# Kernel optimization log

Hardware: AMD Instinct MI355X
Metric: run time of the kernel (lower is better)

Reference implementation:

```python
import jax, jax.numpy as jnp
import numpy as np

N = 50000      # nodes
E = 1600000    # edges (avg degree 32)
F_IN = 512     # num_node_features
NHID = 128     # args.nhid
NCLS = 64      # num_classes


def _gcn_conv(x, W, b, src, dst):
    """PyG GCNConv with symmetric normalization and self-loops.
    x' = D^{-1/2} (A + I) D^{-1/2} (x W) + b, D = degree of (A + I)."""
    h = x @ W                                   # [N, d_out] linear first
    ones = jnp.ones(src.shape[0], h.dtype)
    deg = jnp.zeros(N, h.dtype).at[dst].add(ones) + 1.0  # +1 for self-loop
    dinv = jax.lax.rsqrt(deg)                   # D^{-1/2}
    norm = dinv[src] * dinv[dst]                # per-edge coefficient
    msg = h[src] * norm[:, None]                # gather + scale  [E, d_out]
    agg = jnp.zeros_like(h).at[dst].add(msg)    # scatter-add
    agg = agg + h * (dinv * dinv)[:, None]      # self-loop term (norm = dinv_i^2)
    return agg + b


def setup_inputs() -> dict:
    key = jax.random.key(0)
    k0, k1, k2, k3, k4, k5 = jax.random.split(key, 6)
    x = jax.random.normal(k0, (N, F_IN), jnp.float32)
    edge_index = jax.random.randint(k1, (2, E), 0, N, jnp.int32)
    W1 = jax.random.normal(k2, (F_IN, NHID), jnp.float32) / np.sqrt(F_IN)
    b1 = jnp.zeros((NHID,), jnp.float32)
    W2 = jax.random.normal(k3, (NHID, NCLS), jnp.float32) / np.sqrt(NHID)
    b2 = jnp.zeros((NCLS,), jnp.float32)
    return {"x": x, "edge_index": edge_index, "W1": W1, "b1": b1, "W2": W2, "b2": b2}


def reference(x, edge_index, W1, b1, W2, b2):
    src, dst = edge_index[0], edge_index[1]
    h = jax.nn.relu(_gcn_conv(x, W1, b1, src, dst))
    # dropout is identity at inference (training=False)
    out = _gcn_conv(h, W2, b2, src, dst)
    return jax.nn.softmax(out, axis=1)
```

## Files before the change

### kernel.cpp

```cpp
#include <hip/hip_runtime.h>
#include <hip/hip_bf16.h>
#include <hip/hip_fp16.h>


#define F_IN 512
#define NHID 128
#define NCLS 64
#define BSHIFT 8
#define CHUNK 4096
#define BM 64
#define BK 32

typedef __attribute__((ext_vector_type(8))) short short8;
typedef __attribute__((ext_vector_type(4))) float f32x4;

__device__ __forceinline__ unsigned f2u(float f) { union { float f; unsigned u; } v; v.f = f; return v.u; }
__device__ __forceinline__ float u2f(unsigned u) { union { unsigned u; float f; } v; v.u = u; return v.f; }


__global__ __launch_bounds__(256) void bin_kernel(const int* __restrict__ src,
        const int* __restrict__ dst, unsigned* __restrict__ pairs,
        int* __restrict__ bcur, int E, int cap) {
    __shared__ int lcnt[256];
    __shared__ int lscan[256];
    __shared__ int gbase[256];
    __shared__ int wsum[4];
    __shared__ unsigned stage[CHUNK];
    const int t = threadIdx.x;
    const int lane = t & 63, wid = t >> 6;
    const int e0 = blockIdx.x * CHUNK;
    const int n = min(CHUNK, E - e0);

    lcnt[t] = 0;
    __syncthreads();
    for (int i = t; i < n; i += 256)
        atomicAdd(&lcnt[dst[e0 + i] >> BSHIFT], 1);
    __syncthreads();
    const int v = lcnt[t];
    int s = v;
    #pragma unroll
    for (int d = 1; d < 64; d <<= 1) {
        int tt = __shfl_up(s, d);
        if (lane >= d) s += tt;
    }
    if (lane == 63) wsum[wid] = s;
    __syncthreads();
    int woff = 0;
    for (int w = 0; w < wid; ++w) woff += wsum[w];
    lscan[t] = woff + s - v;
    gbase[t] = v ? atomicAdd(&bcur[t], v) : 0;
    lcnt[t] = 0;
    __syncthreads();
    for (int i = t; i < n; i += 256) {
        unsigned d = (unsigned)dst[e0 + i], sc = (unsigned)src[e0 + i];
        int b = d >> BSHIFT;
        int p = atomicAdd(&lcnt[b], 1);
        stage[lscan[b] + p] = (d << 16) | sc;
    }
    __syncthreads();
    for (int i = t; i < n; i += 256) {
        unsigned pr = stage[i];
        int b = pr >> 24;
        int off = gbase[b] + (i - lscan[b]);
        if (off < cap) pairs[(size_t)b * cap + off] = pr;
    }
}


__global__ __launch_bounds__(256) void scanB_kernel(const int* __restrict__ bcur,
        int* __restrict__ bbase, int nbuck, int cap) {
    __shared__ int wsum[4];
    const int t = threadIdx.x;
    const int lane = t & 63, wid = t >> 6;
    int v = (t < nbuck) ? min(bcur[t], cap) : 0;
    int s = v;
    #pragma unroll
    for (int d = 1; d < 64; d <<= 1) {
        int tt = __shfl_up(s, d);
        if (lane >= d) s += tt;
    }
    if (lane == 63) wsum[wid] = s;
    __syncthreads();
    int woff = 0;
    for (int w = 0; w < wid; ++w) woff += wsum[w];
    bbase[t] = woff + s - v;
}


__global__ __launch_bounds__(512) void countscan_b_kernel(
        const unsigned* __restrict__ pairs, const int* __restrict__ bcur,
        const int* __restrict__ bbase, int* __restrict__ row_ptr,
        float* __restrict__ dinv, int cap, int N) {
    __shared__ int hist[256];
    __shared__ int wsum[4];
    const int b = blockIdx.x;
    const int t = threadIdx.x;
    if (t < 256) hist[t] = 0;
    __syncthreads();
    const int n = min(bcur[b], cap);
    const unsigned* p = pairs + (size_t)b * cap;
    for (int i = t; i < n; i += 512)
        atomicAdd(&hist[(p[i] >> 16) & 255], 1);
    __syncthreads();
    if (t < 256) {
        const int lane = t & 63, wid = t >> 6;
        const int v = hist[t];
        int s = v;
        #pragma unroll
        for (int d = 1; d < 64; d <<= 1) {
            int tt = __shfl_up(s, d);
            if (lane >= d) s += tt;
        }
        if (lane == 63) wsum[wid] = s;
        __syncthreads();
        int woff = 0;
        for (int w = 0; w < wid; ++w) woff += wsum[w];
        const int excl = woff + s - v;
        const int node = (b << BSHIFT) + t;
        if (node <= N) row_ptr[node] = bbase[b] + excl;
        if (node < N) dinv[node] = rsqrtf((float)v + 1.0f);
    }
}


__global__ __launch_bounds__(1024) void fill_b_kernel(const unsigned* __restrict__ pairs,
        const int* __restrict__ bcur, const int* __restrict__ row_ptr,
        int* __restrict__ col, int cap) {
    __shared__ int lcur[256];
    const int b = blockIdx.x;
    const int t = threadIdx.x;
    if (t < 256) lcur[t] = 0;
    __syncthreads();
    const int n = min(bcur[b], cap);
    const unsigned* p = pairs + (size_t)b * cap;
    for (int i = t; i < n; i += 1024) {
        unsigned pr = p[i];
        int dl = (pr >> 16) & 255;
        int pos = row_ptr[(b << BSHIFT) + dl] + atomicAdd(&lcur[dl], 1);
        col[pos] = (int)(pr & 0xffffu);
    }
}


__global__ __launch_bounds__(256) void prepW_kernel(const float* __restrict__ W1,
        short* __restrict__ Wp) {
    const int g = blockIdx.x * 256 + threadIdx.x;
    const int f = g >> 6;
    const int lane = g & 63;
    const int ks = f >> 3, nt = f & 7;
    const int colg = nt * 16 + (lane & 15);
    const int k0 = ks * 32 + (lane >> 4) * 8;
    short8 vb;
    #pragma unroll
    for (int j = 0; j < 8; ++j) {
        unsigned u = f2u(W1[(size_t)(k0 + j) * NHID + colg]);
        unsigned r = (u + 0x7fffu + ((u >> 16) & 1u)) >> 16;
        vb[j] = (short)r;
    }
    *reinterpret_cast<short8*>(Wp + ((size_t)f << 9) + (lane << 3)) = vb;
}


__device__ __forceinline__ void cvt8v(const f32x4& u0, const f32x4& u1,
                                      short8& h, short8& l) {
    float av[8] = {u0[0], u0[1], u0[2], u0[3], u1[0], u1[1], u1[2], u1[3]};
    #pragma unroll
    for (int j = 0; j < 8; ++j) {
        unsigned u = f2u(av[j]);
        h[j] = (short)(u >> 16);
        float hif = u2f(u & 0xffff0000u);
        l[j] = (short)(f2u(av[j] - hif) >> 16);
    }
}

#define STAGE(bufidx, ksv) do { \
    const char* _xb = (const char*)X + (size_t)(ksv) * 128; \
    char* _ab = (char*)&Abuf[bufidx][0] + tid * 16; \
    __builtin_amdgcn_global_load_lds((const unsigned*)(_xb + aoff0), (unsigned*)(_ab),        16, 0, 0); \
    __builtin_amdgcn_global_load_lds((const unsigned*)(_xb + aoff1), (unsigned*)(_ab + 4096), 16, 0, 0); \
    const char* _wb = (const char*)Wp + (size_t)(ksv) * 8192 + tid * 16; \
    char* _bb = (char*)&Bbuf[bufidx][0] + tid * 16; \
    __builtin_amdgcn_global_load_lds((const unsigned*)(_wb),        (unsigned*)(_bb),        16, 0, 0); \
    __builtin_amdgcn_global_load_lds((const unsigned*)(_wb + 4096), (unsigned*)(_bb + 4096), 16, 0, 0); \
} while (0)

__global__ __launch_bounds__(256, 4) void gemm1_mfma(
        const float* __restrict__ X, const short* __restrict__ Wp,
        const float* __restrict__ dinv, __half* __restrict__ Hs16, int M) {
    __shared__ float Abuf[2][BM * BK];
    __shared__ short Bbuf[2][8 * 512];
    const int tid = threadIdx.x;
    const int lane = tid & 63;
    const int wid = tid >> 6;
    const int l15 = lane & 15;
    const int kc = lane >> 4;
    const int m0 = blockIdx.x * BM;

    int aoff0, aoff1;
    {
        int o, row, c, grow;
        o = tid * 16;        row = o >> 7; c = ((o >> 4) & 7) ^ (row & 7);
        grow = m0 + row; if (grow > M - 1) grow = M - 1; aoff0 = grow * 2048 + c * 16;
        o = 4096 + tid * 16; row = o >> 7; c = ((o >> 4) & 7) ^ (row & 7);
        grow = m0 + row; if (grow > M - 1) grow = M - 1; aoff1 = grow * 2048 + c * 16;
    }

    const int row0 = wid * 16 + l15;
    const int ra0 = row0 * 128 + (((kc * 2) ^ (row0 & 7)) * 16);
    const int ra1 = row0 * 128 + (((kc * 2 + 1) ^ (row0 & 7)) * 16);

    f32x4 acc[8];
    #pragma unroll
    for (int j = 0; j < 8; ++j)
        acc[j] = (f32x4){0.f, 0.f, 0.f, 0.f};

    STAGE(0, 0);
    __syncthreads();

    for (int ks = 0; ks < 16; ++ks) {
        const int cur = ks & 1;
        if (ks + 1 < 16) STAGE(cur ^ 1, ks + 1);
        const char* ab = (const char*)&Abuf[cur][0];
        const f32x4 x0 = *reinterpret_cast<const f32x4*>(ab + ra0);
        const f32x4 x1 = *reinterpret_cast<const f32x4*>(ab + ra1);
        short8 ah, al;
        cvt8v(x0, x1, ah, al);
        const char* bb = (const char*)&Bbuf[cur][0];
        short8 bfr[8];
        #pragma unroll
        for (int nt = 0; nt < 8; ++nt)
            bfr[nt] = *reinterpret_cast<const short8*>(bb + nt * 1024 + lane * 16);
        #pragma unroll
        for (int nt = 0; nt < 8; ++nt) {
            acc[nt] = __builtin_amdgcn_mfma_f32_16x16x32_bf16(ah, bfr[nt], acc[nt], 0, 0, 0);
            acc[nt] = __builtin_amdgcn_mfma_f32_16x16x32_bf16(al, bfr[nt], acc[nt], 0, 0, 0);
        }
        __syncthreads();
    }

    #pragma unroll
    for (int r = 0; r < 4; ++r) {
        const int orow = m0 + wid * 16 + kc * 4 + r;
        if (orow < M) {
            const float di = dinv[orow];
            #pragma unroll
            for (int nt = 0; nt < 8; ++nt) {
                Hs16[(size_t)orow * NHID + nt * 16 + l15] =
                    __float2half(acc[nt][r] * di);
            }
        }
    }
}


__global__ __launch_bounds__(64) void agg1_kernel(const __half2* __restrict__ Hs,
        const int* __restrict__ row_ptr, const int* __restrict__ col,
        const float* __restrict__ dinv, const float* __restrict__ b1,
        float* __restrict__ Y) {
    const int i = blockIdx.x;
    const int c = threadIdx.x;
    const int beg = row_ptr[i], end = row_ptr[i + 1];
    float2 f = __half22float2(Hs[(size_t)i * 64 + c]);
    float ax = f.x, ay = f.y;
    int e = beg;
    for (; e + 8 <= end; e += 8) {
        float2 v[8];
        #pragma unroll
        for (int j = 0; j < 8; ++j) {
            int s = col[e + j];
            v[j] = __half22float2(Hs[(size_t)s * 64 + c]);
        }
        #pragma unroll
        for (int j = 0; j < 8; ++j) { ax += v[j].x; ay += v[j].y; }
    }
    for (; e < end; ++e) {
        float2 v = __half22float2(Hs[(size_t)col[e] * 64 + c]);
        ax += v.x; ay += v.y;
    }
    const float di = dinv[i];
    const float2 bb = reinterpret_cast<const float2*>(b1)[c];
    float2 o;
    o.x = fmaxf(fmaf(ax, di, bb.x), 0.0f);
    o.y = fmaxf(fmaf(ay, di, bb.y), 0.0f);
    *reinterpret_cast<float2*>(&Y[(size_t)i * NHID + 2 * c]) = o;
}


__global__ __launch_bounds__(256) void gemm2_kernel(const float* __restrict__ Y,
        const float* __restrict__ W2, const float* __restrict__ dinv,
        __half* __restrict__ H2s16, int N) {
    __shared__ float Ws[NHID][NCLS];
    __shared__ float Ys[16][NHID];
    const int tid = threadIdx.x;
    const int i0 = blockIdx.x * 16;
    #pragma unroll
    for (int t = 0; t < 8; ++t) {
        int v = tid + t * 256;
        int k = v >> 4;
        int c4 = (v & 15) * 4;
        *reinterpret_cast<float4*>(&Ws[k][c4]) =
            *reinterpret_cast<const float4*>(&W2[(size_t)k * NCLS + c4]);
    }
    #pragma unroll
    for (int t = 0; t < 2; ++t) {
        int v = tid + t * 256;
        int r = v >> 5;
        int c4 = (v & 31) * 4;
        int gr = i0 + r; if (gr > N - 1) gr = N - 1;
        *reinterpret_cast<float4*>(&Ys[r][c4]) =
            *reinterpret_cast<const float4*>(&Y[(size_t)gr * NHID + c4]);
    }
    __syncthreads();
    const int c = tid & 63;
    const int rg = tid >> 6;
    float acc[4] = {0.f, 0.f, 0.f, 0.f};
    #pragma unroll 8
    for (int k = 0; k < NHID; ++k) {
        float w = Ws[k][c];
        #pragma unroll
        for (int j = 0; j < 4; ++j)
            acc[j] = fmaf(Ys[rg * 4 + j][k], w, acc[j]);
    }
    #pragma unroll
    for (int j = 0; j < 4; ++j) {
        int gr = i0 + rg * 4 + j;
        if (gr < N) H2s16[(size_t)gr * NCLS + c] = __float2half(acc[j] * dinv[gr]);
    }
}


__global__ __launch_bounds__(64) void agg2_kernel(const __half2* __restrict__ H2,
        const int* __restrict__ row_ptr, const int* __restrict__ col,
        const float* __restrict__ dinv, const float* __restrict__ b2,
        float* __restrict__ out, int N) {
    const int lane = threadIdx.x;
    const int node = blockIdx.x * 2 + (lane >> 5);
    const int c = lane & 31;
    if (node >= N) return;
    const int beg = row_ptr[node], end = row_ptr[node + 1];
    float2 f = __half22float2(H2[(size_t)node * 32 + c]);
    float ax = f.x, ay = f.y;
    int e = beg;
    for (; e + 8 <= end; e += 8) {
        float2 v[8];
        #pragma unroll
        for (int j = 0; j < 8; ++j) {
            int s = col[e + j];
            v[j] = __half22float2(H2[(size_t)s * 32 + c]);
        }
        #pragma unroll
        for (int j = 0; j < 8; ++j) { ax += v[j].x; ay += v[j].y; }
    }
    for (; e < end; ++e) {
        float2 v = __half22float2(H2[(size_t)col[e] * 32 + c]);
        ax += v.x; ay += v.y;
    }
    const float di = dinv[node];
    const float2 bb = reinterpret_cast<const float2*>(b2)[c];
    float vx = fmaf(ax, di, bb.x);
    float vy = fmaf(ay, di, bb.y);
    float m = fmaxf(vx, vy);
    #pragma unroll
    for (int d = 16; d >= 1; d >>= 1) m = fmaxf(m, __shfl_xor(m, d));
    float ex = __expf(vx - m), ey = __expf(vy - m);
    float sum = ex + ey;
    #pragma unroll
    for (int d = 16; d >= 1; d >>= 1) sum += __shfl_xor(sum, d);
    float2 o = {ex / sum, ey / sum};
    reinterpret_cast<float2*>(out)[(size_t)node * 32 + c] = o;
}


extern "C" void kernel_launch(void* const* d_in, const int* in_sizes, int n_in,
                              void* d_out, int out_size, void* d_ws, size_t ws_size,
                              hipStream_t stream) {
    const float* x  = (const float*)d_in[0];
    const int*   ei = (const int*)d_in[1];
    const float* W1 = (const float*)d_in[2];
    const float* b1 = (const float*)d_in[3];
    const float* W2 = (const float*)d_in[4];
    const float* b2 = (const float*)d_in[5];
    const int N = in_sizes[0] / F_IN;
    const int E = in_sizes[1] / 2;
    const int* src = ei;
    const int* dst = ei + E;
    float* out = (float*)d_out;

    const int Npad  = (N + 63) & ~63;
    const int Epad  = (E + 63) & ~63;
    int*      bcur    = (int*)d_ws;
    int*      bbase   = bcur + 256;
    int*      row_ptr = bbase + 256;
    float*    dinv    = (float*)(row_ptr + Npad);
    int*      col     = (int*)(dinv + Npad);
    __half*   Hs16    = (__half*)(col + Epad);
    float*    Y       = (float*)(Hs16 + (size_t)Npad * NHID);
    __half*   H2s16   = Hs16;
    short*    Wp      = (short*)Y;
    unsigned* pairs   = (unsigned*)((char*)Y + 512 * 1024);

    const int nbuck = (N + 255) >> BSHIFT;
    const int cap = (((E / nbuck) * 3 / 2) + 63) & ~63;

    hipMemsetAsync(bcur, 0, 256 * sizeof(int), stream);
    bin_kernel<<<(E + CHUNK - 1) / CHUNK, 256, 0, stream>>>(src, dst, pairs, bcur, E, cap);
    scanB_kernel<<<1, 256, 0, stream>>>(bcur, bbase, nbuck, cap);
    countscan_b_kernel<<<nbuck, 512, 0, stream>>>(pairs, bcur, bbase, row_ptr, dinv, cap, N);
    fill_b_kernel<<<nbuck, 1024, 0, stream>>>(pairs, bcur, row_ptr, col, cap);
    prepW_kernel<<<32, 256, 0, stream>>>(W1, Wp);
    gemm1_mfma<<<(N + BM - 1) / BM, 256, 0, stream>>>(x, Wp, dinv, Hs16, N);
    agg1_kernel<<<N, 64, 0, stream>>>((const __half2*)Hs16, row_ptr, col, dinv, b1, Y);
    gemm2_kernel<<<(N + 15) / 16, 256, 0, stream>>>(Y, W2, dinv, H2s16, N);
    agg2_kernel<<<(N + 1) / 2, 64, 0, stream>>>((const __half2*)H2s16, row_ptr, col, dinv, b2, out, N);
}
```

Before: 175.6 us.

## Fuse CSR bucket scan, count and fill; store hidden activations in fp16

Merges the bucket-offset scan, per-bucket count/scan and fill kernels into one kernel. Each block now computes its own bucket base with a reduction over earlier bucket counts and reuses the shared-memory scan for the column placement, which removes two launches and the global row_ptr reads. Separately, the layer-1 output Y is stored as half2 instead of fp32, halving the write and re-read traffic between agg1 and gemm2, at the cost of reduced precision. The workspace layout changes so that Y16, Wp and pairs no longer alias.

```diff
diff --git a/kernel.cpp b/kernel.cpp
--- a/kernel.cpp
+++ b/kernel.cpp
@@ -67,76 +67,62 @@
 }
 
 
-__global__ __launch_bounds__(256) void scanB_kernel(const int* __restrict__ bcur,
-        int* __restrict__ bbase, int nbuck, int cap) {
-    __shared__ int wsum[4];
-    const int t = threadIdx.x;
-    const int lane = t & 63, wid = t >> 6;
-    int v = (t < nbuck) ? min(bcur[t], cap) : 0;
-    int s = v;
-    #pragma unroll
-    for (int d = 1; d < 64; d <<= 1) {
-        int tt = __shfl_up(s, d);
-        if (lane >= d) s += tt;
-    }
-    if (lane == 63) wsum[wid] = s;
-    __syncthreads();
-    int woff = 0;
-    for (int w = 0; w < wid; ++w) woff += wsum[w];
-    bbase[t] = woff + s - v;
-}
-
-
-__global__ __launch_bounds__(512) void countscan_b_kernel(
+__global__ __launch_bounds__(1024) void countfill_b_kernel(
         const unsigned* __restrict__ pairs, const int* __restrict__ bcur,
-        const int* __restrict__ bbase, int* __restrict__ row_ptr,
-        float* __restrict__ dinv, int cap, int N) {
+        int* __restrict__ row_ptr, float* __restrict__ dinv,
+        int* __restrict__ col, int cap, int N) {
     __shared__ int hist[256];
+    __shared__ int lscan[256];
+    __shared__ int red[16];
     __shared__ int wsum[4];
     const int b = blockIdx.x;
     const int t = threadIdx.x;
+    const int lane = t & 63, wv = t >> 6;
+
+    int bv = (t < 256 && t < b) ? min(bcur[t], cap) : 0;
+    #pragma unroll
+    for (int d = 32; d >= 1; d >>= 1) bv += __shfl_xor(bv, d);
+    if (lane == 0) red[wv] = bv;
     if (t < 256) hist[t] = 0;
     __syncthreads();
+    int bbase = 0;
+    #pragma unroll
+    for (int w = 0; w < 16; ++w) bbase += red[w];
+
     const int n = min(bcur[b], cap);
     const unsigned* p = pairs + (size_t)b * cap;
-    for (int i = t; i < n; i += 512)
+    for (int i = t; i < n; i += 1024)
         atomicAdd(&hist[(p[i] >> 16) & 255], 1);
     __syncthreads();
+
+    int s = 0, v2 = 0;
     if (t < 256) {
-        const int lane = t & 63, wid = t >> 6;
-        const int v = hist[t];
-        int s = v;
+        v2 = hist[t];
+        s = v2;
         #pragma unroll
         for (int d = 1; d < 64; d <<= 1) {
             int tt = __shfl_up(s, d);
             if (lane >= d) s += tt;
         }
-        if (lane == 63) wsum[wid] = s;
-        __syncthreads();
+        if (lane == 63) wsum[wv] = s;
+    }
+    __syncthreads();
+    if (t < 256) {
         int woff = 0;
-        for (int w = 0; w < wid; ++w) woff += wsum[w];
-        const int excl = woff + s - v;
+        for (int w = 0; w < wv; ++w) woff += wsum[w];
+        const int excl = woff + s - v2;
+        lscan[t] = excl;
         const int node = (b << BSHIFT) + t;
-        if (node <= N) row_ptr[node] = bbase[b] + excl;
-        if (node < N) dinv[node] = rsqrtf((float)v + 1.0f);
-    }
-}
-
-
-__global__ __launch_bounds__(1024) void fill_b_kernel(const unsigned* __restrict__ pairs,
-        const int* __restrict__ bcur, const int* __restrict__ row_ptr,
-        int* __restrict__ col, int cap) {
-    __shared__ int lcur[256];
-    const int b = blockIdx.x;
-    const int t = threadIdx.x;
-    if (t < 256) lcur[t] = 0;
-    __syncthreads();
-    const int n = min(bcur[b], cap);
-    const unsigned* p = pairs + (size_t)b * cap;
+        if (node <= N) row_ptr[node] = bbase + excl;
+        if (node < N) dinv[node] = rsqrtf((float)v2 + 1.0f);
+    }
+    __syncthreads();
+    if (t < 256) hist[t] = 0;
+    __syncthreads();
     for (int i = t; i < n; i += 1024) {
         unsigned pr = p[i];
         int dl = (pr >> 16) & 255;
-        int pos = row_ptr[(b << BSHIFT) + dl] + atomicAdd(&lcur[dl], 1);
+        int pos = bbase + lscan[dl] + atomicAdd(&hist[dl], 1);
         col[pos] = (int)(pr & 0xffffu);
     }
 }
@@ -256,7 +242,7 @@
 __global__ __launch_bounds__(64) void agg1_kernel(const __half2* __restrict__ Hs,
         const int* __restrict__ row_ptr, const int* __restrict__ col,
         const float* __restrict__ dinv, const float* __restrict__ b1,
-        float* __restrict__ Y) {
+        __half2* __restrict__ Y16) {
     const int i = blockIdx.x;
     const int c = threadIdx.x;
     const int beg = row_ptr[i], end = row_ptr[i + 1];
@@ -279,18 +265,17 @@
     }
     const float di = dinv[i];
     const float2 bb = reinterpret_cast<const float2*>(b1)[c];
-    float2 o;
-    o.x = fmaxf(fmaf(ax, di, bb.x), 0.0f);
-    o.y = fmaxf(fmaf(ay, di, bb.y), 0.0f);
-    *reinterpret_cast<float2*>(&Y[(size_t)i * NHID + 2 * c]) = o;
-}
-
-
-__global__ __launch_bounds__(256) void gemm2_kernel(const float* __restrict__ Y,
+    float ox = fmaxf(fmaf(ax, di, bb.x), 0.0f);
+    float oy = fmaxf(fmaf(ay, di, bb.y), 0.0f);
+    Y16[(size_t)i * 64 + c] = __floats2half2_rn(ox, oy);
+}
+
+
+__global__ __launch_bounds__(256) void gemm2_kernel(const __half2* __restrict__ Y16,
         const float* __restrict__ W2, const float* __restrict__ dinv,
         __half* __restrict__ H2s16, int N) {
     __shared__ float Ws[NHID][NCLS];
-    __shared__ float Ys[16][NHID];
+    __shared__ __half2 Ys2[16][NCLS];
     const int tid = threadIdx.x;
     const int i0 = blockIdx.x * 16;
     #pragma unroll
@@ -301,25 +286,26 @@
         *reinterpret_cast<float4*>(&Ws[k][c4]) =
             *reinterpret_cast<const float4*>(&W2[(size_t)k * NCLS + c4]);
     }
-    #pragma unroll
-    for (int t = 0; t < 2; ++t) {
-        int v = tid + t * 256;
-        int r = v >> 5;
-        int c4 = (v & 31) * 4;
+    {
+        int r = tid >> 4;
+        int c4 = (tid & 15) * 4;
         int gr = i0 + r; if (gr > N - 1) gr = N - 1;
-        *reinterpret_cast<float4*>(&Ys[r][c4]) =
-            *reinterpret_cast<const float4*>(&Y[(size_t)gr * NHID + c4]);
+        *reinterpret_cast<float4*>(&Ys2[r][c4]) =
+            *reinterpret_cast<const float4*>(&Y16[(size_t)gr * 64 + c4]);
     }
     __syncthreads();
     const int c = tid & 63;
     const int rg = tid >> 6;
     float acc[4] = {0.f, 0.f, 0.f, 0.f};
     #pragma unroll 8
-    for (int k = 0; k < NHID; ++k) {
-        float w = Ws[k][c];
-        #pragma unroll
-        for (int j = 0; j < 4; ++j)
-            acc[j] = fmaf(Ys[rg * 4 + j][k], w, acc[j]);
+    for (int kp = 0; kp < 64; ++kp) {
+        const float w0 = Ws[2 * kp][c];
+        const float w1 = Ws[2 * kp + 1][c];
+        #pragma unroll
+        for (int j = 0; j < 4; ++j) {
+            float2 y2 = __half22float2(Ys2[rg * 4 + j][kp]);
+            acc[j] = fmaf(y2.x, w0, fmaf(y2.y, w1, acc[j]));
+        }
     }
     #pragma unroll
     for (int j = 0; j < 4; ++j) {
@@ -388,28 +374,25 @@
 
     const int Npad  = (N + 63) & ~63;
     const int Epad  = (E + 63) & ~63;
+    const int nbuck = (N + 255) >> BSHIFT;
+    const int cap = (((E / nbuck) * 3 / 2) + 63) & ~63;
+
     int*      bcur    = (int*)d_ws;
-    int*      bbase   = bcur + 256;
-    int*      row_ptr = bbase + 256;
+    int*      row_ptr = bcur + 256;
     float*    dinv    = (float*)(row_ptr + Npad);
     int*      col     = (int*)(dinv + Npad);
     __half*   Hs16    = (__half*)(col + Epad);
-    float*    Y       = (float*)(Hs16 + (size_t)Npad * NHID);
+    __half2*  Y16     = (__half2*)(Hs16 + (size_t)Npad * NHID);
+    short*    Wp      = (short*)(Y16 + (size_t)Npad * 64);
+    unsigned* pairs   = (unsigned*)(Wp + 65536);
     __half*   H2s16   = Hs16;
-    short*    Wp      = (short*)Y;
-    unsigned* pairs   = (unsigned*)((char*)Y + 512 * 1024);
-
-    const int nbuck = (N + 255) >> BSHIFT;
-    const int cap = (((E / nbuck) * 3 / 2) + 63) & ~63;
 
     hipMemsetAsync(bcur, 0, 256 * sizeof(int), stream);
     bin_kernel<<<(E + CHUNK - 1) / CHUNK, 256, 0, stream>>>(src, dst, pairs, bcur, E, cap);
-    scanB_kernel<<<1, 256, 0, stream>>>(bcur, bbase, nbuck, cap);
-    countscan_b_kernel<<<nbuck, 512, 0, stream>>>(pairs, bcur, bbase, row_ptr, dinv, cap, N);
-    fill_b_kernel<<<nbuck, 1024, 0, stream>>>(pairs, bcur, row_ptr, col, cap);
+    countfill_b_kernel<<<nbuck, 1024, 0, stream>>>(pairs, bcur, row_ptr, dinv, col, cap, N);
     prepW_kernel<<<32, 256, 0, stream>>>(W1, Wp);
     gemm1_mfma<<<(N + BM - 1) / BM, 256, 0, stream>>>(x, Wp, dinv, Hs16, N);
-    agg1_kernel<<<N, 64, 0, stream>>>((const __half2*)Hs16, row_ptr, col, dinv, b1, Y);
-    gemm2_kernel<<<(N + 15) / 16, 256, 0, stream>>>(Y, W2, dinv, H2s16, N);
+    agg1_kernel<<<N, 64, 0, stream>>>((const __half2*)Hs16, row_ptr, col, dinv, b1, Y16);
+    gemm2_kernel<<<(N + 15) / 16, 256, 0, stream>>>(Y16, W2, dinv, H2s16, N);
     agg2_kernel<<<(N + 1) / 2, 64, 0, stream>>>((const __half2*)H2s16, row_ptr, col, dinv, b2, out, N);
 }
```

After: 168.9 us. 1.04x faster.
